# Kernel tuning notes

Measured on AMD Instinct MI355X. Metric: run time of the kernel, lower is better.

## Reference

```python
import jax, jax.numpy as jnp
import numpy as np


def setup_inputs() -> dict:
    key = jax.random.key(0)
    k1, k2, k3, k4 = jax.random.split(key, 4)
    B, N, Fin, Fout, K = 8, 256, 64, 64, 3
    H = jax.random.normal(k1, (B, N, N, Fin), dtype=jnp.float32)
    # static Chebyshev polynomial stacks T_0..T_{K-1} for origin / dest Laplacians
    cheb_L1 = jax.random.normal(k2, (K, N, N), dtype=jnp.float32) * 0.1
    cheb_L2 = jax.random.normal(k3, (K, N, N), dtype=jnp.float32) * 0.1
    # xavier_uniform over last two dims (fan_in=Fin, fan_out=Fout)
    limit = float(np.sqrt(6.0 / (Fin + Fout)))
    weights = jax.random.uniform(k4, (K, K, Fin, Fout), dtype=jnp.float32,
                                 minval=-limit, maxval=limit)
    bias = jnp.zeros((Fout,), dtype=jnp.float32)
    return {"H": H, "cheb_L1": cheb_L1, "cheb_L2": cheb_L2,
            "weights": weights, "bias": bias}


def reference(H, cheb_L1, cheb_L2, weights, bias):
    # H' = relu( sum_{i,j} T_i(L1) @_1 H @_2 T_j(L2) @_3 W_ij + b )
    # Step 1: left graph shift for all i at once: (K,B,N,N,F)
    H_x1 = jnp.einsum('kuv,bvwf->kbuwf', cheb_L1, H)
    # Step 2+3 fused: right shift by T_j, project by W_ij, accumulate over i,j
    out = jnp.einsum('kbuwf,lwz,klfo->buzo', H_x1, cheb_L2, weights)
    return jax.nn.relu(out + bias)
```

## Files before the change

kernel.cpp:

```cpp
#include <hip/hip_runtime.h>

typedef __attribute__((ext_vector_type(8))) short s16x8;
typedef __attribute__((ext_vector_type(4))) float f32x4;

#define MFMA16 __builtin_amdgcn_mfma_f32_16x16x32_bf16
#define WAIT_VM0() asm volatile("s_waitcnt vmcnt(0)" ::: "memory")

__device__ __forceinline__ short f2bf(float x) {
  union { float f; unsigned u; } c; c.f = x;
  unsigned r = (c.u + 0x7fffu + ((c.u >> 16) & 1u)) >> 16;
  return (short)r;
}

__device__ __forceinline__ void gld16(const void* g, void* l) {
  __builtin_amdgcn_global_load_lds(
      (const __attribute__((address_space(1))) unsigned*)g,
      (__attribute__((address_space(3))) unsigned*)l, 16, 0, 0);
}


__global__ __launch_bounds__(256) void k_cvt_l1(const float* __restrict__ L1,
                                                short* __restrict__ L1b) {
  int i = blockIdx.x * 256 + threadIdx.x;
  L1b[i] = f2bf(L1[i]);
}

__global__ __launch_bounds__(256) void k_build_l2cat(const float* __restrict__ L2,
                                                     short* __restrict__ L2cat) {
  __shared__ float t[32][33];
  const int l = blockIdx.z, w0 = blockIdx.x * 32, z0 = blockIdx.y * 32;
  const int tx = threadIdx.x, ty = threadIdx.y;
  const float* src = L2 + (size_t)l * 65536;
  for (int i = ty; i < 32; i += 8) t[i][tx] = src[(size_t)(w0 + i) * 256 + z0 + tx];
  __syncthreads();
  for (int i = ty; i < 32; i += 8)
    L2cat[(size_t)(z0 + i) * 768 + l * 256 + w0 + tx] = f2bf(t[tx][i]);
}

__global__ __launch_bounds__(256) void k_build_wt(const float* __restrict__ W,
                                                  short* __restrict__ WT) {
  for (int idx = threadIdx.x + blockIdx.x * 256; idx < 192 * 192; idx += 256 * gridDim.x) {
    int lo = idx / 192, kf = idx % 192;
    int l = lo >> 6, o = lo & 63, k = kf / 64, f = kf & 63;
    WT[idx] = f2bf(W[(((size_t)(k * 3 + l) * 64 + f) << 6) + o]);
  }
}

__global__ __launch_bounds__(256) void k_cvt_ht(const float* __restrict__ H,
                                                short* __restrict__ HbT, int b0) {
  __shared__ float t[32][33];
  const int bc = blockIdx.z;
  const int wf0 = blockIdx.x * 32, v0 = blockIdx.y * 32;
  const int tx = threadIdx.x, ty = threadIdx.y;
  const float* src = H + ((size_t)(b0 + bc) * 256 + v0) * 16384;
  for (int i = ty; i < 32; i += 8) t[i][tx] = src[(size_t)i * 16384 + wf0 + tx];
  __syncthreads();
  short* dst = HbT + ((size_t)bc * 16384 + wf0) * 256;
  for (int i = ty; i < 32; i += 8) dst[(size_t)i * 256 + v0 + tx] = f2bf(t[tx][i]);
}

__global__ __launch_bounds__(256, 4) void k_s1(const short* __restrict__ L1b,
                                               const short* __restrict__ HbT,
                                               short* __restrict__ A2) {
  __shared__ __align__(16) short At[2][128 * 32];
  __shared__ __align__(16) short Bt[2][128 * 32];
  const int t = threadIdx.x, lane = t & 63, wid = t >> 6;
  const int n0 = blockIdx.x * 128;
  const int kk = blockIdx.y >> 1;
  const int u0 = (blockIdx.y & 1) * 128;
  const int bc = blockIdx.z;
  const short* Ag = L1b + (size_t)kk * 65536;
  const short* Bg = HbT + (size_t)bc * 16384 * 256;
  const int wm = wid >> 1, wn = wid & 1;
  const int srow = lane >> 2;
  const int selem = ((lane & 3) ^ ((lane >> 3) & 3)) * 8;
  const int koff = ((lane >> 4) ^ ((lane >> 1) & 3)) * 8;
  const int ar = lane & 15;
#pragma unroll
  for (int j = 0; j < 2; ++j) {
    const int rb = wid * 32 + j * 16;
    gld16(Ag + (size_t)(u0 + rb + srow) * 256 + selem, At[0] + rb * 32);
    gld16(Bg + (size_t)(n0 + rb + srow) * 256 + selem, Bt[0] + rb * 32);
  }
  __syncthreads();
  f32x4 acc[4][4] = {};
#pragma unroll
  for (int kt8 = 0; kt8 < 8; ++kt8) {
    const int cur = kt8 & 1;
    s16x8 a[4], b[4];
#pragma unroll
    for (int i = 0; i < 4; ++i)
      a[i] = *(const s16x8*)&At[cur][(wm * 64 + i * 16 + ar) * 32 + koff];
#pragma unroll
    for (int j = 0; j < 4; ++j)
      b[j] = *(const s16x8*)&Bt[cur][(wn * 64 + j * 16 + ar) * 32 + koff];
    if (kt8 < 7) {
#pragma unroll
      for (int j = 0; j < 2; ++j) {
        const int rb = wid * 32 + j * 16;
        gld16(Ag + (size_t)(u0 + rb + srow) * 256 + (kt8 + 1) * 32 + selem, At[cur ^ 1] + rb * 32);
        gld16(Bg + (size_t)(n0 + rb + srow) * 256 + (kt8 + 1) * 32 + selem, Bt[cur ^ 1] + rb * 32);
      }
    }
#pragma unroll
    for (int i = 0; i < 4; ++i)
#pragma unroll
      for (int j = 0; j < 4; ++j) acc[i][j] = MFMA16(a[i], b[j], acc[i][j], 0, 0, 0);
    __syncthreads();
  }
  const int cr = lane >> 4, cc = lane & 15;
#pragma unroll
  for (int i = 0; i < 4; ++i)
#pragma unroll
    for (int j = 0; j < 4; ++j) {
      const int ncol = n0 + wn * 64 + j * 16 + cc;
      const int w = ncol >> 6, f = ncol & 63;
#pragma unroll
      for (int r = 0; r < 4; ++r) {
        const int u = u0 + wm * 64 + i * 16 + cr * 4 + r;
        A2[(((size_t)bc * 256 + u) * 256 + w) * 192 + kk * 64 + f] = f2bf(acc[i][j][r]);
      }
    }
}

__global__ __launch_bounds__(512, 4) void k_s23(const short* __restrict__ A2,
                                                const short* __restrict__ WTg,
                                                const short* __restrict__ L2cat,
                                                const float* __restrict__ bias,
                                                float* __restrict__ out, int b0) {
  __shared__ __align__(16) char lds[81920];
  short* P   = (short*)lds;
  short* Ws  = (short*)lds;
  short* AtS = (short*)(lds + 49152);
  const int t = threadIdx.x, lane = t & 63, wid = t >> 6;
  const int bx = blockIdx.x;
  const int bul = (bx & 7) | ((bx >> 4) << 3);
  const int o0 = ((bx >> 3) & 1) * 32;
  const int ar = lane & 15, cc = ar, cr = lane >> 4, sl = lane & 7;
  const int srow = lane >> 2;
  const int selem = ((lane & 3) ^ ((lane >> 3) & 3)) * 8;
  const int koff = ((lane >> 4) ^ ((lane >> 1) & 3)) * 8;
  const short* A2g = A2 + (size_t)bul * 49152;

  for (int s = wid; s < 36; s += 8) {
    const int t6 = s / 6, rb = (s % 6) * 16;
    const int gr = (rb >> 5) * 64 + o0 + (rb & 31);
    gld16(WTg + (size_t)(gr + srow) * 192 + t6 * 32 + selem, Ws + (t6 * 96 + rb) * 32);
  }
#pragma unroll
  for (int is = 0; is < 2; ++is)
    gld16(A2g + (size_t)(wid * 32 + is * 16 + srow) * 192 + selem,
          AtS + (wid * 32 + is * 16) * 32);
  __syncthreads();

  f32x4 acc[3][2][2] = {};
#pragma unroll
  for (int kt6 = 0; kt6 < 6; ++kt6) {
    const int cur = kt6 & 1;
    WAIT_VM0();
    s16x8 a[2];
#pragma unroll
    for (int i = 0; i < 2; ++i)
      a[i] = *(const s16x8*)&AtS[(cur * 256 + wid * 32 + i * 16 + ar) * 32 + koff];
    s16x8 b[3][2];
#pragma unroll
    for (int l = 0; l < 3; ++l)
#pragma unroll
      for (int j = 0; j < 2; ++j)
        b[l][j] = *(const s16x8*)&Ws[(kt6 * 96 + l * 32 + j * 16 + ar) * 32 + koff];
    if (kt6 < 5) {
#pragma unroll
      for (int is = 0; is < 2; ++is)
        gld16(A2g + (size_t)(wid * 32 + is * 16 + srow) * 192 + (kt6 + 1) * 32 + selem,
              AtS + ((cur ^ 1) * 256 + wid * 32 + is * 16) * 32);
    }
#pragma unroll
    for (int l = 0; l < 3; ++l)
#pragma unroll
      for (int j = 0; j < 2; ++j)
#pragma unroll
        for (int i = 0; i < 2; ++i)
          acc[l][j][i] = MFMA16(a[i], b[l][j], acc[l][j][i], 0, 0, 0);
  }

  __syncthreads();

#pragma unroll
  for (int l = 0; l < 3; ++l)
#pragma unroll
    for (int j = 0; j < 2; ++j)
#pragma unroll
      for (int i = 0; i < 2; ++i)
#pragma unroll
        for (int rp = 0; rp < 2; ++rp) {
          const int r = rp * 2;
          const int w = wid * 32 + i * 16 + cr * 4 + r;
          const int o = j * 16 + cc;
          const int lw = l * 256 + w;
          const int addr = o * 768 + ((lw >> 3) ^ (o & 7)) * 8 + (lw & 7);
          unsigned lo16 = (unsigned short)f2bf(acc[l][j][i][r]);
          unsigned hi16 = (unsigned short)f2bf(acc[l][j][i][r + 1]);
          *(unsigned*)&P[addr] = lo16 | (hi16 << 16);
        }
#pragma unroll
  for (int is = 0; is < 2; ++is)
    gld16(L2cat + (size_t)(wid * 32 + is * 16 + srow) * 768 + selem,
          AtS + (wid * 32 + is * 16) * 32);
  __syncthreads();

  f32x4 acc2[2][2] = {};
#pragma unroll
  for (int t2 = 0; t2 < 24; ++t2) {
    const int cur = t2 & 1;
    const int kt = t2 * 32;
    WAIT_VM0();
    s16x8 a[2], b[2];
#pragma unroll
    for (int i = 0; i < 2; ++i)
      a[i] = *(const s16x8*)&AtS[(cur * 256 + wid * 32 + i * 16 + ar) * 32 + koff];
#pragma unroll
    for (int j = 0; j < 2; ++j) {
      const int S = (kt >> 3) + (lane >> 4);
      b[j] = *(const s16x8*)&P[(j * 16 + ar) * 768 + (S ^ sl) * 8];
    }
    if (t2 < 23) {
#pragma unroll
      for (int is = 0; is < 2; ++is)
        gld16(L2cat + (size_t)(wid * 32 + is * 16 + srow) * 768 + (t2 + 1) * 32 + selem,
              AtS + ((cur ^ 1) * 256 + wid * 32 + is * 16) * 32);
    }
#pragma unroll
    for (int i = 0; i < 2; ++i)
#pragma unroll
      for (int j = 0; j < 2; ++j) acc2[i][j] = MFMA16(a[i], b[j], acc2[i][j], 0, 0, 0);
  }

  float* og = out + ((size_t)b0 * 256 + bul) * 16384;
#pragma unroll
  for (int i = 0; i < 2; ++i)
#pragma unroll
    for (int j = 0; j < 2; ++j) {
      const float bv = bias[o0 + j * 16 + cc];
#pragma unroll
      for (int r = 0; r < 4; ++r) {
        const int z = wid * 32 + i * 16 + cr * 4 + r;
        og[(size_t)z * 64 + o0 + j * 16 + cc] = fmaxf(acc2[i][j][r] + bv, 0.f);
      }
    }
}

extern "C" void kernel_launch(void* const* d_in, const int* in_sizes, int n_in,
                              void* d_out, int out_size, void* d_ws, size_t ws_size,
                              hipStream_t stream) {
  const float* H    = (const float*)d_in[0];
  const float* L1   = (const float*)d_in[1];
  const float* L2   = (const float*)d_in[2];
  const float* W    = (const float*)d_in[3];
  const float* bias = (const float*)d_in[4];
  float* out = (float*)d_out;

  char* ws = (char*)d_ws;
  short* L1b   = (short*)ws;
  short* L2cat = (short*)(ws + (384 << 10));
  short* WT    = (short*)(ws + (768 << 10));
  char* data = ws + (4ull << 20);

  const size_t perb = 32ull << 20;
  size_t avail = (ws_size > (4ull << 20)) ? ws_size - (4ull << 20) : 0;
  int nb = 1;
  if (avail >= 8 * perb) nb = 8;
  else if (avail >= 4 * perb) nb = 4;
  else if (avail >= 2 * perb) nb = 2;

  short* HbT = (short*)data;
  short* A2  = (short*)(data + (size_t)nb * (8ull << 20));

  k_cvt_l1<<<768, 256, 0, stream>>>(L1, L1b);
  k_build_l2cat<<<dim3(8, 8, 3), dim3(32, 8), 0, stream>>>(L2, L2cat);
  k_build_wt<<<36, 256, 0, stream>>>(W, WT);

  for (int b0 = 0; b0 < 8; b0 += nb) {
    k_cvt_ht<<<dim3(512, 8, nb), dim3(32, 8), 0, stream>>>(H, HbT, b0);
    k_s1<<<dim3(128, 6, nb), 256, 0, stream>>>(L1b, HbT, A2);
    k_s23<<<nb * 512, 512, 0, stream>>>(A2, WT, L2cat, bias, out, b0);
  }
}
```

Measured before the change: 352.1 us.

## Store stage-1 output in MFMA fragment layout and load operands directly into registers

Stage 1 now writes its bf16 result in a layout grouped by MFMA k-slice, so stage 2/3 can read the A fragments straight from global memory into registers instead of staging them through LDS. The L2cat operand in the final GEMM is likewise loaded directly into registers, using a three-deep software prefetch ring. LDS usage falls from 80 KB to 48 KB, which may allow more resident blocks, and the per-step vmcnt waits and LDS round-trips go away. In exchange, k_s1's stores become more scattered, and more global-load latency must be hidden by the register prefetch, which raises register pressure.

```diff
diff --git a/kernel.cpp b/kernel.cpp
--- a/kernel.cpp
+++ b/kernel.cpp
@@ -4,7 +4,6 @@
 typedef __attribute__((ext_vector_type(4))) float f32x4;
 
 #define MFMA16 __builtin_amdgcn_mfma_f32_16x16x32_bf16
-#define WAIT_VM0() asm volatile("s_waitcnt vmcnt(0)" ::: "memory")
 
 __device__ __forceinline__ short f2bf(float x) {
   union { float f; unsigned u; } c; c.f = x;
@@ -61,7 +60,7 @@
 
 __global__ __launch_bounds__(256, 4) void k_s1(const short* __restrict__ L1b,
                                                const short* __restrict__ HbT,
-                                               short* __restrict__ A2) {
+                                               short* __restrict__ A2F) {
   __shared__ __align__(16) short At[2][128 * 32];
   __shared__ __align__(16) short Bt[2][128 * 32];
   const int t = threadIdx.x, lane = t & 63, wid = t >> 6;
@@ -115,75 +114,76 @@
     for (int j = 0; j < 4; ++j) {
       const int ncol = n0 + wn * 64 + j * 16 + cc;
       const int w = ncol >> 6, f = ncol & 63;
+      const int kt6 = kk * 2 + (f >> 5), ksw = (f >> 3) & 3, f7 = f & 7;
+      const int off = ((kt6 * 4 + ksw) * 256 + w) * 8 + f7;
 #pragma unroll
       for (int r = 0; r < 4; ++r) {
         const int u = u0 + wm * 64 + i * 16 + cr * 4 + r;
-        A2[(((size_t)bc * 256 + u) * 256 + w) * 192 + kk * 64 + f] = f2bf(acc[i][j][r]);
-      }
-    }
-}
-
-__global__ __launch_bounds__(512, 4) void k_s23(const short* __restrict__ A2,
+        A2F[(size_t)(bc * 256 + u) * 49152 + off] = f2bf(acc[i][j][r]);
+      }
+    }
+}
+
+__global__ __launch_bounds__(512, 4) void k_s23(const short* __restrict__ A2F,
                                                 const short* __restrict__ WTg,
                                                 const short* __restrict__ L2cat,
                                                 const float* __restrict__ bias,
                                                 float* __restrict__ out, int b0) {
-  __shared__ __align__(16) char lds[81920];
-  short* P   = (short*)lds;
-  short* Ws  = (short*)lds;
-  short* AtS = (short*)(lds + 49152);
+  __shared__ __align__(16) short P[32 * 768];
+  short* Ws = P;
   const int t = threadIdx.x, lane = t & 63, wid = t >> 6;
   const int bx = blockIdx.x;
   const int bul = (bx & 7) | ((bx >> 4) << 3);
   const int o0 = ((bx >> 3) & 1) * 32;
-  const int ar = lane & 15, cc = ar, cr = lane >> 4, sl = lane & 7;
+  const int ar = lane & 15, cc = ar, cr = lane >> 4, sl = lane & 7, ks = lane >> 4;
   const int srow = lane >> 2;
   const int selem = ((lane & 3) ^ ((lane >> 3) & 3)) * 8;
   const int koff = ((lane >> 4) ^ ((lane >> 1) & 3)) * 8;
-  const short* A2g = A2 + (size_t)bul * 49152;
-
+  const short* A2g = A2F + (size_t)bul * 49152;
+
+#define ALOAD(kt6, i) \
+  (*(const s16x8*)&A2g[(((kt6) * 4 + ks) * 256 + wid * 32 + (i) * 16 + ar) * 8])
+#define ZLOAD(t2, i) \
+  (*(const s16x8*)&L2cat[(size_t)(wid * 32 + (i) * 16 + ar) * 768 + (t2) * 32 + ks * 8])
+
+  s16x8 apf0[2], apf1[2], apf2[2];
+  apf0[0] = ALOAD(0, 0); apf0[1] = ALOAD(0, 1);
+  apf1[0] = ALOAD(1, 0); apf1[1] = ALOAD(1, 1);
+  apf2[0] = ALOAD(2, 0); apf2[1] = ALOAD(2, 1);
   for (int s = wid; s < 36; s += 8) {
     const int t6 = s / 6, rb = (s % 6) * 16;
     const int gr = (rb >> 5) * 64 + o0 + (rb & 31);
     gld16(WTg + (size_t)(gr + srow) * 192 + t6 * 32 + selem, Ws + (t6 * 96 + rb) * 32);
   }
-#pragma unroll
-  for (int is = 0; is < 2; ++is)
-    gld16(A2g + (size_t)(wid * 32 + is * 16 + srow) * 192 + selem,
-          AtS + (wid * 32 + is * 16) * 32);
   __syncthreads();
 
   f32x4 acc[3][2][2] = {};
 #pragma unroll
   for (int kt6 = 0; kt6 < 6; ++kt6) {
-    const int cur = kt6 & 1;
-    WAIT_VM0();
-    s16x8 a[2];
-#pragma unroll
-    for (int i = 0; i < 2; ++i)
-      a[i] = *(const s16x8*)&AtS[(cur * 256 + wid * 32 + i * 16 + ar) * 32 + koff];
-    s16x8 b[3][2];
+    s16x8 a0, a1;
+    if (kt6 % 3 == 0)      { a0 = apf0[0]; a1 = apf0[1]; }
+    else if (kt6 % 3 == 1) { a0 = apf1[0]; a1 = apf1[1]; }
+    else                   { a0 = apf2[0]; a1 = apf2[1]; }
+    if (kt6 < 3) {
+      if (kt6 % 3 == 0)      { apf0[0] = ALOAD(kt6 + 3, 0); apf0[1] = ALOAD(kt6 + 3, 1); }
+      else if (kt6 % 3 == 1) { apf1[0] = ALOAD(kt6 + 3, 0); apf1[1] = ALOAD(kt6 + 3, 1); }
+      else                   { apf2[0] = ALOAD(kt6 + 3, 0); apf2[1] = ALOAD(kt6 + 3, 1); }
+    }
 #pragma unroll
     for (int l = 0; l < 3; ++l)
 #pragma unroll
-      for (int j = 0; j < 2; ++j)
-        b[l][j] = *(const s16x8*)&Ws[(kt6 * 96 + l * 32 + j * 16 + ar) * 32 + koff];
-    if (kt6 < 5) {
-#pragma unroll
-      for (int is = 0; is < 2; ++is)
-        gld16(A2g + (size_t)(wid * 32 + is * 16 + srow) * 192 + (kt6 + 1) * 32 + selem,
-              AtS + ((cur ^ 1) * 256 + wid * 32 + is * 16) * 32);
-    }
-#pragma unroll
-    for (int l = 0; l < 3; ++l)
-#pragma unroll
-      for (int j = 0; j < 2; ++j)
-#pragma unroll
-        for (int i = 0; i < 2; ++i)
-          acc[l][j][i] = MFMA16(a[i], b[l][j], acc[l][j][i], 0, 0, 0);
-  }
-
-  __syncthreads();
+      for (int j = 0; j < 2; ++j) {
+        s16x8 b = *(const s16x8*)&Ws[(kt6 * 96 + l * 32 + j * 16 + ar) * 32 + koff];
+        acc[l][j][0] = MFMA16(a0, b, acc[l][j][0], 0, 0, 0);
+        acc[l][j][1] = MFMA16(a1, b, acc[l][j][1], 0, 0, 0);
+      }
+  }
+  __syncthreads();
+
+  s16x8 zpf0[2], zpf1[2], zpf2[2];
+  zpf0[0] = ZLOAD(0, 0); zpf0[1] = ZLOAD(0, 1);
+  zpf1[0] = ZLOAD(1, 0); zpf1[1] = ZLOAD(1, 1);
+  zpf2[0] = ZLOAD(2, 0); zpf2[1] = ZLOAD(2, 1);
 
 #pragma unroll
   for (int l = 0; l < 3; ++l)
@@ -196,44 +196,38 @@
           const int r = rp * 2;
           const int w = wid * 32 + i * 16 + cr * 4 + r;
           const int o = j * 16 + cc;
+          const int lw0 = 0 * 256 + w, lw1 = 256 + w, lw2 = 512 + w;
+          (void)lw1; (void)lw2;
           const int lw = l * 256 + w;
           const int addr = o * 768 + ((lw >> 3) ^ (o & 7)) * 8 + (lw & 7);
           unsigned lo16 = (unsigned short)f2bf(acc[l][j][i][r]);
           unsigned hi16 = (unsigned short)f2bf(acc[l][j][i][r + 1]);
           *(unsigned*)&P[addr] = lo16 | (hi16 << 16);
         }
-#pragma unroll
-  for (int is = 0; is < 2; ++is)
-    gld16(L2cat + (size_t)(wid * 32 + is * 16 + srow) * 768 + selem,
-          AtS + (wid * 32 + is * 16) * 32);
   __syncthreads();
 
   f32x4 acc2[2][2] = {};
 #pragma unroll
   for (int t2 = 0; t2 < 24; ++t2) {
-    const int cur = t2 & 1;
-    const int kt = t2 * 32;
-    WAIT_VM0();
-    s16x8 a[2], b[2];
-#pragma unroll
-    for (int i = 0; i < 2; ++i)
-      a[i] = *(const s16x8*)&AtS[(cur * 256 + wid * 32 + i * 16 + ar) * 32 + koff];
-#pragma unroll
-    for (int j = 0; j < 2; ++j) {
-      const int S = (kt >> 3) + (lane >> 4);
-      b[j] = *(const s16x8*)&P[(j * 16 + ar) * 768 + (S ^ sl) * 8];
-    }
-    if (t2 < 23) {
-#pragma unroll
-      for (int is = 0; is < 2; ++is)
-        gld16(L2cat + (size_t)(wid * 32 + is * 16 + srow) * 768 + (t2 + 1) * 32 + selem,
-              AtS + ((cur ^ 1) * 256 + wid * 32 + is * 16) * 32);
-    }
-#pragma unroll
-    for (int i = 0; i < 2; ++i)
-#pragma unroll
-      for (int j = 0; j < 2; ++j) acc2[i][j] = MFMA16(a[i], b[j], acc2[i][j], 0, 0, 0);
-  }
+    s16x8 a0, a1;
+    if (t2 % 3 == 0)      { a0 = zpf0[0]; a1 = zpf0[1]; }
+    else if (t2 % 3 == 1) { a0 = zpf1[0]; a1 = zpf1[1]; }
+    else                  { a0 = zpf2[0]; a1 = zpf2[1]; }
+    if (t2 < 21) {
+      if (t2 % 3 == 0)      { zpf0[0] = ZLOAD(t2 + 3, 0); zpf0[1] = ZLOAD(t2 + 3, 1); }
+      else if (t2 % 3 == 1) { zpf1[0] = ZLOAD(t2 + 3, 0); zpf1[1] = ZLOAD(t2 + 3, 1); }
+      else                  { zpf2[0] = ZLOAD(t2 + 3, 0); zpf2[1] = ZLOAD(t2 + 3, 1); }
+    }
+    const int S = t2 * 4 + ks;
+    s16x8 b0 = *(const s16x8*)&P[(0 * 16 + ar) * 768 + (S ^ sl) * 8];
+    s16x8 b1 = *(const s16x8*)&P[(1 * 16 + ar) * 768 + (S ^ sl) * 8];
+    acc2[0][0] = MFMA16(a0, b0, acc2[0][0], 0, 0, 0);
+    acc2[0][1] = MFMA16(a0, b1, acc2[0][1], 0, 0, 0);
+    acc2[1][0] = MFMA16(a1, b0, acc2[1][0], 0, 0, 0);
+    acc2[1][1] = MFMA16(a1, b1, acc2[1][1], 0, 0, 0);
+  }
+#undef ALOAD
+#undef ZLOAD
 
   float* og = out + ((size_t)b0 * 256 + bul) * 16384;
 #pragma unroll
@@ -273,7 +267,7 @@
   else if (avail >= 2 * perb) nb = 2;
 
   short* HbT = (short*)data;
-  short* A2  = (short*)(data + (size_t)nb * (8ull << 20));
+  short* A2F = (short*)(data + (size_t)nb * (8ull << 20));
 
   k_cvt_l1<<<768, 256, 0, stream>>>(L1, L1b);
   k_build_l2cat<<<dim3(8, 8, 3), dim3(32, 8), 0, stream>>>(L2, L2cat);
@@ -281,7 +275,7 @@
 
   for (int b0 = 0; b0 < 8; b0 += nb) {
     k_cvt_ht<<<dim3(512, 8, nb), dim3(32, 8), 0, stream>>>(H, HbT, b0);
-    k_s1<<<dim3(128, 6, nb), 256, 0, stream>>>(L1b, HbT, A2);
-    k_s23<<<nb * 512, 512, 0, stream>>>(A2, WT, L2cat, bias, out, b0);
-  }
-}
+    k_s1<<<dim3(128, 6, nb), 256, 0, stream>>>(L1b, HbT, A2F);
+    k_s23<<<nb * 512, 512, 0, stream>>>(A2F, WT, L2cat, bias, out, b0);
+  }
+}
```

New measurement: 493.3 us. +40.1%, slower.
